# Optimization experiments

Hardware: AMD Instinct MI355X
Metric: run time of the kernel (lower is better)

## Reference

```python
import jax, jax.numpy as jnp
import numpy as np

EPS = 1e-5  # torch BatchNorm2d default eps


def setup_inputs() -> dict:
    key = jax.random.key(0)
    ks = jax.random.split(key, 11)
    n, c, h, w = 16, 512, 64, 64
    grp, cg, mip = 4, 128, 16
    return {
        "x": jax.random.normal(ks[0], (n, c, h, w), dtype=jnp.float32),
        "W1": jax.random.normal(ks[1], (mip, cg), dtype=jnp.float32) * 0.05,
        "b1": jax.random.normal(ks[2], (mip,), dtype=jnp.float32) * 0.05,
        "gamma": jax.random.uniform(ks[3], (mip,), dtype=jnp.float32, minval=0.5, maxval=1.5),
        "beta": jax.random.normal(ks[4], (mip,), dtype=jnp.float32) * 0.05,
        "mean": jax.random.normal(ks[5], (mip,), dtype=jnp.float32) * 0.05,
        "var": jax.random.uniform(ks[6], (mip,), dtype=jnp.float32, minval=0.5, maxval=1.5),
        "Wh": jax.random.normal(ks[7], (cg, mip), dtype=jnp.float32) * 0.1,
        "bh": jax.random.normal(ks[8], (cg,), dtype=jnp.float32) * 0.05,
        "Ww": jax.random.normal(ks[9], (cg, mip), dtype=jnp.float32) * 0.1,
        "bw": jax.random.normal(ks[10], (cg,), dtype=jnp.float32) * 0.05,
    }


def reference(x, W1, b1, gamma, beta, mean, var, Wh, bh, Ww, bw):
    n, c, h, w = x.shape
    grp = 4
    cg = c // grp
    # Since c % 4 == 0, torch.split gives 4 equal groups: fold group into a new axis.
    xg = x.reshape(n, grp, cg, h, w)                       # (n,g,cg,h,w)
    gh = xg.mean(axis=4)                                   # pool over w -> (n,g,cg,h)
    gw = xg.mean(axis=3)                                   # pool over h -> (n,g,cg,w)
    y = jnp.concatenate([gh, gw], axis=3)                  # (n,g,cg,h+w)
    # conv1 (1x1) shared across all 4 groups
    y = jnp.einsum('ngcl,mc->ngml', y, W1) + b1[None, None, :, None]
    # BatchNorm2d (eval mode, running stats)
    scale = gamma / jnp.sqrt(var + EPS)
    y = y * scale[None, None, :, None] + (beta - mean * scale)[None, None, :, None]
    # h_swish: x * relu6(x+3)/6
    y = y * (jnp.clip(y + 3.0, 0.0, 6.0) / 6.0)
    yh, yw = y[..., :h], y[..., h:]                        # (n,g,mip,h), (n,g,mip,w)
    a_h = jax.nn.sigmoid(jnp.einsum('ngml,cm->ngcl', yh, Wh) + bh[None, None, :, None])
    a_w = jax.nn.sigmoid(jnp.einsum('ngml,cm->ngcl', yw, Ww) + bw[None, None, :, None])
    out = xg * a_h[..., :, None] * a_w[..., None, :]       # (n,g,cg,h,w)
    out = out.reshape(n, c, h, w)
    # channel shuffle: (n, cg, grp, h, w) -> permute group axis forward
    out = out.reshape(n, cg, grp, h, w).transpose(0, 2, 1, 3, 4).reshape(n, c, h, w)
    return out
```

## Files before the change

### kernel.cpp

```cpp
#include <hip/hip_runtime.h>

#define N_   16
#define C_   512
#define H_   64
#define W_   64
#define GRP  4
#define CG   128
#define MIP  16

__device__ __forceinline__ float bf_lo(unsigned u) { return __uint_as_float(u << 16); }
__device__ __forceinline__ float bf_hi(unsigned u) { return __uint_as_float(u & 0xFFFF0000u); }
__device__ __forceinline__ float bf1(unsigned short s) { return __uint_as_float((unsigned)s << 16); }

__device__ __forceinline__ float ld_scalar(const void* p, int i, bool isbf) {
    return isbf ? bf1(((const unsigned short*)p)[i]) : ((const float*)p)[i];
}

__device__ __forceinline__ bool sniff_isbf(const unsigned* __restrict__ x32,
                                           int t, unsigned* s_flag) {
    if (t < 64) {
        int cnt = 0;
        #pragma unroll
        for (int k = 0; k < 4; ++k) {
            unsigned w = x32[t + 64 * k];
            unsigned e = (w >> 7) & 0xFFu;
            cnt += (e >= 0x60u && e <= 0x9Fu) ? 1 : 0;
        }
        #pragma unroll
        for (int off = 32; off > 0; off >>= 1) cnt += __shfl_down(cnt, off, 64);
        if (t == 0) *s_flag = (cnt >= 192) ? 1u : 0u;
    }
    __syncthreads();
    return *s_flag != 0u;
}

__global__ __launch_bounds__(256) void kreduce(const void* __restrict__ xv,
                                               float* __restrict__ gh,
                                               float* __restrict__ gw) {
    __shared__ float tile[64 * 65];
    __shared__ unsigned flag_s;
    const int bid = blockIdx.x;
    const int t = threadIdx.x;
    const bool isbf = sniff_isbf((const unsigned*)xv, t, &flag_s);

    if (isbf) {
        const uint4* src = (const uint4*)((const unsigned short*)xv + (size_t)bid * 4096);
        #pragma unroll
        for (int half = 0; half < 2; ++half) {
            int idx = t + half * 256;
            int r = idx >> 3;
            int j0 = (idx & 7) * 8;
            uint4 v = src[idx];
            unsigned uu[4] = {v.x, v.y, v.z, v.w};
            #pragma unroll
            for (int k = 0; k < 4; ++k) {
                tile[r * 65 + j0 + 2 * k]     = bf_lo(uu[k]);
                tile[r * 65 + j0 + 2 * k + 1] = bf_hi(uu[k]);
            }
        }
    } else {
        const float4* src = (const float4*)((const float*)xv + (size_t)bid * 4096);
        #pragma unroll
        for (int it = 0; it < 4; ++it) {
            int idx = t + it * 256;
            int r = idx >> 4;
            int j0 = (idx & 15) * 4;
            float4 v = src[idx];
            tile[r * 65 + j0]     = v.x;
            tile[r * 65 + j0 + 1] = v.y;
            tile[r * 65 + j0 + 2] = v.z;
            tile[r * 65 + j0 + 3] = v.w;
        }
    }
    __syncthreads();

    if (t < 64) {
        float s = 0.f;
        #pragma unroll
        for (int j = 0; j < 64; ++j) s += tile[t * 65 + j];
        gh[(size_t)bid * 64 + t] = s * (1.0f / 64.0f);
    } else if (t < 128) {
        int j = t - 64;
        float s = 0.f;
        #pragma unroll
        for (int i = 0; i < 64; ++i) s += tile[i * 65 + j];
        gw[(size_t)bid * 64 + j] = s * (1.0f / 64.0f);
    }
}

__global__ __launch_bounds__(256) void ky(
    const void* __restrict__ xv,
    const float* __restrict__ gh, const float* __restrict__ gw,
    const void* __restrict__ W1, const void* __restrict__ b1,
    const void* __restrict__ gamma, const void* __restrict__ beta,
    const void* __restrict__ mean, const void* __restrict__ var,
    float* __restrict__ y)
{
    __shared__ float W1_s[MIP * CG];
    __shared__ float scale_s[MIP], shift_s[MIP], b1_s[MIP];
    __shared__ unsigned flag_s;

    const int t = threadIdx.x;
    const bool isbf = sniff_isbf((const unsigned*)xv, t, &flag_s);

    if (isbf) {
        uint4 v = ((const uint4*)W1)[t];
        unsigned uu[4] = {v.x, v.y, v.z, v.w};
        #pragma unroll
        for (int k = 0; k < 4; ++k) {
            W1_s[t * 8 + 2 * k]     = bf_lo(uu[k]);
            W1_s[t * 8 + 2 * k + 1] = bf_hi(uu[k]);
        }
    } else {
        #pragma unroll
        for (int it = 0; it < 2; ++it) {
            int idx = t + 256 * it;
            float4 v = ((const float4*)W1)[idx];
            W1_s[idx * 4]     = v.x;
            W1_s[idx * 4 + 1] = v.y;
            W1_s[idx * 4 + 2] = v.z;
            W1_s[idx * 4 + 3] = v.w;
        }
    }
    if (t < MIP) {
        float sc = ld_scalar(gamma, t, isbf) * rsqrtf(ld_scalar(var, t, isbf) + 1e-5f);
        scale_s[t] = sc;
        shift_s[t] = ld_scalar(beta, t, isbf) - ld_scalar(mean, t, isbf) * sc;
        b1_s[t] = ld_scalar(b1, t, isbf);
    }
    __syncthreads();

    const int l = t & 127;
    const int half = t >> 7;
    const size_t base = (size_t)blockIdx.x * (CG * 64);
    const float* src = (l < 64) ? (gh + base + l) : (gw + base + (l - 64));
    float acc[8] = {0.f, 0.f, 0.f, 0.f, 0.f, 0.f, 0.f, 0.f};
    for (int cc = 0; cc < CG; ++cc) {
        float v = src[(size_t)cc * 64];
        #pragma unroll
        for (int mm = 0; mm < 8; ++mm)
            acc[mm] += W1_s[(half * 8 + mm) * CG + cc] * v;
    }
    float* yb = y + (size_t)blockIdx.x * (MIP * 128);
    #pragma unroll
    for (int mm = 0; mm < 8; ++mm) {
        int m = half * 8 + mm;
        float yv = acc[mm] + b1_s[m];
        yv = yv * scale_s[m] + shift_s[m];
        float hc = fminf(fmaxf(yv + 3.0f, 0.0f), 6.0f);
        yb[m * 128 + l] = yv * hc * (1.0f / 6.0f);
    }
}

__global__ __launch_bounds__(256) void kapply(const void* __restrict__ xv,
                                              const float* __restrict__ y,
                                              const void* __restrict__ Wh,
                                              const void* __restrict__ bh,
                                              const void* __restrict__ Ww,
                                              const void* __restrict__ bw,
                                              void* __restrict__ outv) {
    __shared__ float ah_s[64], aw_s[64];
    __shared__ unsigned flag_s;
    const int bid = blockIdx.x;
    const int n = bid >> 9;
    const int o = bid & 511;
    const int g2 = o >> 7, cc2 = o & 127;
    const int p = cc2 * 4 + g2;
    const int g = p >> 7, cc = p & 127;
    const int t = threadIdx.x;
    const bool isbf = sniff_isbf((const unsigned*)xv, t, &flag_s);

    if (t < 128) {
        const int i = t & 63;
        const bool isW = (t >= 64);
        const void* Wp = isW ? Ww : Wh;
        const void* bp = isW ? bw : bh;
        const float* ysrc = y + (size_t)(n * 4 + g) * (MIP * 128) + (isW ? 64 : 0) + i;
        float acc = ld_scalar(bp, cc, isbf);
        #pragma unroll
        for (int m = 0; m < MIP; ++m)
            acc += ld_scalar(Wp, cc * MIP + m, isbf) * ysrc[m * 128];
        float s = 1.0f / (1.0f + __expf(-acc));
        if (isW) aw_s[i] = s; else ah_s[i] = s;
    }
    __syncthreads();

    if (isbf) {
        const uint4* src = (const uint4*)((const unsigned short*)xv + ((size_t)n * 512 + p) * 4096);
        uint4* dst = (uint4*)((unsigned short*)outv + (size_t)bid * 4096);
        #pragma unroll
        for (int half = 0; half < 2; ++half) {
            int idx = t + half * 256;
            int r = idx >> 3;
            int j0 = (idx & 7) * 8;
            float sah = ah_s[r];
            uint4 v = src[idx];
            unsigned uu[4] = {v.x, v.y, v.z, v.w};
            unsigned res[4];
            #pragma unroll
            for (int k = 0; k < 4; ++k) {
                int j = j0 + 2 * k;
                float f0 = bf_lo(uu[k]) * sah * aw_s[j];
                float f1 = bf_hi(uu[k]) * sah * aw_s[j + 1];
                unsigned u0 = __float_as_uint(f0); u0 += 0x7FFFu + ((u0 >> 16) & 1u);
                unsigned u1 = __float_as_uint(f1); u1 += 0x7FFFu + ((u1 >> 16) & 1u);
                res[k] = (u0 >> 16) | (u1 & 0xFFFF0000u);
            }
            uint4 w; w.x = res[0]; w.y = res[1]; w.z = res[2]; w.w = res[3];
            dst[idx] = w;
        }
    } else {
        const float4* src = (const float4*)((const float*)xv + ((size_t)n * 512 + p) * 4096);
        float4* dst = (float4*)((float*)outv + (size_t)bid * 4096);
        #pragma unroll
        for (int it = 0; it < 4; ++it) {
            int idx = t + it * 256;
            int r = idx >> 4;
            int j0 = (idx & 15) * 4;
            float sah = ah_s[r];
            float4 v = src[idx];
            v.x *= sah * aw_s[j0];
            v.y *= sah * aw_s[j0 + 1];
            v.z *= sah * aw_s[j0 + 2];
            v.w *= sah * aw_s[j0 + 3];
            dst[idx] = v;
        }
    }
}

extern "C" void kernel_launch(void* const* d_in, const int* in_sizes, int n_in,
                              void* d_out, int out_size, void* d_ws, size_t ws_size,
                              hipStream_t stream) {
    const void* x     = d_in[0];
    const void* W1    = d_in[1];
    const void* b1    = d_in[2];
    const void* gamma = d_in[3];
    const void* beta  = d_in[4];
    const void* mean  = d_in[5];
    const void* var   = d_in[6];
    const void* Wh    = d_in[7];
    const void* bh    = d_in[8];
    const void* Ww    = d_in[9];
    const void* bw    = d_in[10];

    float* ws = (float*)d_ws;
    const size_t seg = (size_t)N_ * GRP * CG * 64;
    float* gh = ws;
    float* gw = gh + seg;
    float* yv = gw + seg;

    kreduce<<<N_ * C_, 256, 0, stream>>>(x, gh, gw);
    ky<<<N_ * GRP, 256, 0, stream>>>(x, gh, gw, W1, b1, gamma, beta, mean, var, yv);
    kapply<<<N_ * C_, 256, 0, stream>>>(x, yv, Wh, bh, Ww, bw, d_out);
}
```

Before: 277.7 us.

## Move attention sigmoid into mid kernel and reduce pools with register shuffles

The reduce kernel now builds row sums with wavefront shuffles and column partials in registers, instead of staging the whole 64x64 tile in shared memory and reducing it serially. The second-stage conv plus sigmoid moves from the apply kernel into the 64-block mid kernel, which writes precomputed a_h/a_w arrays, so each apply block only loads 128 floats. The apply kernel also issues its x loads before the barrier to overlap them with the attention fetch. The mid kernel now does more serial work on only 64 blocks, which could lengthen that stage.

After: 291.1 us. 4.8% more time.

```diff
diff --git a/kernel.cpp b/kernel.cpp
--- a/kernel.cpp
+++ b/kernel.cpp
@@ -2,8 +2,6 @@
 
 #define N_   16
 #define C_   512
-#define H_   64
-#define W_   64
 #define GRP  4
 #define CG   128
 #define MIP  16
@@ -37,7 +35,7 @@
 __global__ __launch_bounds__(256) void kreduce(const void* __restrict__ xv,
                                                float* __restrict__ gh,
                                                float* __restrict__ gw) {
-    __shared__ float tile[64 * 65];
+    __shared__ float scratch[32][65];
     __shared__ unsigned flag_s;
     const int bid = blockIdx.x;
     const int t = threadIdx.x;
@@ -45,62 +43,74 @@
 
     if (isbf) {
         const uint4* src = (const uint4*)((const unsigned short*)xv + (size_t)bid * 4096);
-        #pragma unroll
-        for (int half = 0; half < 2; ++half) {
-            int idx = t + half * 256;
+        float cp[8] = {0,0,0,0,0,0,0,0};
+        #pragma unroll
+        for (int hf = 0; hf < 2; ++hf) {
+            int idx = t + hf * 256;
             int r = idx >> 3;
-            int j0 = (idx & 7) * 8;
             uint4 v = src[idx];
             unsigned uu[4] = {v.x, v.y, v.z, v.w};
+            float rp = 0.f;
             #pragma unroll
             for (int k = 0; k < 4; ++k) {
-                tile[r * 65 + j0 + 2 * k]     = bf_lo(uu[k]);
-                tile[r * 65 + j0 + 2 * k + 1] = bf_hi(uu[k]);
+                float f0 = bf_lo(uu[k]), f1 = bf_hi(uu[k]);
+                rp += f0 + f1;
+                cp[2*k] += f0; cp[2*k+1] += f1;
             }
-        }
+            rp += __shfl_xor(rp, 1);
+            rp += __shfl_xor(rp, 2);
+            rp += __shfl_xor(rp, 4);
+            if ((t & 7) == 0) gh[(size_t)bid * 64 + r] = rp * (1.f/64.f);
+        }
+        #pragma unroll
+        for (int k = 0; k < 8; ++k) scratch[t >> 3][(t & 7) * 8 + k] = cp[k];
     } else {
         const float4* src = (const float4*)((const float*)xv + (size_t)bid * 4096);
+        float cp[4] = {0,0,0,0};
         #pragma unroll
         for (int it = 0; it < 4; ++it) {
             int idx = t + it * 256;
             int r = idx >> 4;
-            int j0 = (idx & 15) * 4;
             float4 v = src[idx];
-            tile[r * 65 + j0]     = v.x;
-            tile[r * 65 + j0 + 1] = v.y;
-            tile[r * 65 + j0 + 2] = v.z;
-            tile[r * 65 + j0 + 3] = v.w;
-        }
-    }
-    __syncthreads();
-
+            float rp = (v.x + v.y) + (v.z + v.w);
+            cp[0] += v.x; cp[1] += v.y; cp[2] += v.z; cp[3] += v.w;
+            rp += __shfl_xor(rp, 1);
+            rp += __shfl_xor(rp, 2);
+            rp += __shfl_xor(rp, 4);
+            rp += __shfl_xor(rp, 8);
+            if ((t & 15) == 0) gh[(size_t)bid * 64 + r] = rp * (1.f/64.f);
+        }
+        #pragma unroll
+        for (int k = 0; k < 4; ++k) scratch[t >> 4][(t & 15) * 4 + k] = cp[k];
+    }
+    __syncthreads();
     if (t < 64) {
+        const int nr = isbf ? 32 : 16;
         float s = 0.f;
-        #pragma unroll
-        for (int j = 0; j < 64; ++j) s += tile[t * 65 + j];
-        gh[(size_t)bid * 64 + t] = s * (1.0f / 64.0f);
-    } else if (t < 128) {
-        int j = t - 64;
-        float s = 0.f;
-        #pragma unroll
-        for (int i = 0; i < 64; ++i) s += tile[i * 65 + j];
-        gw[(size_t)bid * 64 + j] = s * (1.0f / 64.0f);
-    }
-}
-
-__global__ __launch_bounds__(256) void ky(
+        for (int i = 0; i < nr; ++i) s += scratch[i][t];
+        gw[(size_t)bid * 64 + t] = s * (1.f/64.f);
+    }
+}
+
+__global__ __launch_bounds__(256) void kmid(
     const void* __restrict__ xv,
     const float* __restrict__ gh, const float* __restrict__ gw,
     const void* __restrict__ W1, const void* __restrict__ b1,
     const void* __restrict__ gamma, const void* __restrict__ beta,
     const void* __restrict__ mean, const void* __restrict__ var,
-    float* __restrict__ y)
+    const void* __restrict__ Wh, const void* __restrict__ bh,
+    const void* __restrict__ Ww, const void* __restrict__ bw,
+    float* __restrict__ aH, float* __restrict__ aW)
 {
     __shared__ float W1_s[MIP * CG];
+    __shared__ float Whw_s[2][CG * MIP];
+    __shared__ float y_s[MIP * 128];
+    __shared__ float bhw_s[2][CG];
     __shared__ float scale_s[MIP], shift_s[MIP], b1_s[MIP];
     __shared__ unsigned flag_s;
 
     const int t = threadIdx.x;
+    const int ng = blockIdx.x;
     const bool isbf = sniff_isbf((const unsigned*)xv, t, &flag_s);
 
     if (isbf) {
@@ -108,20 +118,37 @@
         unsigned uu[4] = {v.x, v.y, v.z, v.w};
         #pragma unroll
         for (int k = 0; k < 4; ++k) {
-            W1_s[t * 8 + 2 * k]     = bf_lo(uu[k]);
-            W1_s[t * 8 + 2 * k + 1] = bf_hi(uu[k]);
+            W1_s[t*8 + 2*k]   = bf_lo(uu[k]);
+            W1_s[t*8 + 2*k+1] = bf_hi(uu[k]);
+        }
+        uint4 a = ((const uint4*)Wh)[t];
+        unsigned ua[4] = {a.x, a.y, a.z, a.w};
+        #pragma unroll
+        for (int k = 0; k < 4; ++k) {
+            Whw_s[0][t*8 + 2*k]   = bf_lo(ua[k]);
+            Whw_s[0][t*8 + 2*k+1] = bf_hi(ua[k]);
+        }
+        uint4 c = ((const uint4*)Ww)[t];
+        unsigned uc[4] = {c.x, c.y, c.z, c.w};
+        #pragma unroll
+        for (int k = 0; k < 4; ++k) {
+            Whw_s[1][t*8 + 2*k]   = bf_lo(uc[k]);
+            Whw_s[1][t*8 + 2*k+1] = bf_hi(uc[k]);
         }
     } else {
         #pragma unroll
         for (int it = 0; it < 2; ++it) {
             int idx = t + 256 * it;
             float4 v = ((const float4*)W1)[idx];
-            W1_s[idx * 4]     = v.x;
-            W1_s[idx * 4 + 1] = v.y;
-            W1_s[idx * 4 + 2] = v.z;
-            W1_s[idx * 4 + 3] = v.w;
-        }
-    }
+            W1_s[idx*4] = v.x; W1_s[idx*4+1] = v.y; W1_s[idx*4+2] = v.z; W1_s[idx*4+3] = v.w;
+            float4 a = ((const float4*)Wh)[idx];
+            Whw_s[0][idx*4] = a.x; Whw_s[0][idx*4+1] = a.y; Whw_s[0][idx*4+2] = a.z; Whw_s[0][idx*4+3] = a.w;
+            float4 c = ((const float4*)Ww)[idx];
+            Whw_s[1][idx*4] = c.x; Whw_s[1][idx*4+1] = c.y; Whw_s[1][idx*4+2] = c.z; Whw_s[1][idx*4+3] = c.w;
+        }
+    }
+    if (t < CG) bhw_s[0][t] = ld_scalar(bh, t, isbf);
+    else        bhw_s[1][t - CG] = ld_scalar(bw, t - CG, isbf);
     if (t < MIP) {
         float sc = ld_scalar(gamma, t, isbf) * rsqrtf(ld_scalar(var, t, isbf) + 1e-5f);
         scale_s[t] = sc;
@@ -130,72 +157,75 @@
     }
     __syncthreads();
 
-    const int l = t & 127;
-    const int half = t >> 7;
-    const size_t base = (size_t)blockIdx.x * (CG * 64);
-    const float* src = (l < 64) ? (gh + base + l) : (gw + base + (l - 64));
-    float acc[8] = {0.f, 0.f, 0.f, 0.f, 0.f, 0.f, 0.f, 0.f};
-    for (int cc = 0; cc < CG; ++cc) {
-        float v = src[(size_t)cc * 64];
-        #pragma unroll
-        for (int mm = 0; mm < 8; ++mm)
-            acc[mm] += W1_s[(half * 8 + mm) * CG + cc] * v;
-    }
-    float* yb = y + (size_t)blockIdx.x * (MIP * 128);
-    #pragma unroll
-    for (int mm = 0; mm < 8; ++mm) {
-        int m = half * 8 + mm;
-        float yv = acc[mm] + b1_s[m];
-        yv = yv * scale_s[m] + shift_s[m];
-        float hc = fminf(fmaxf(yv + 3.0f, 0.0f), 6.0f);
-        yb[m * 128 + l] = yv * hc * (1.0f / 6.0f);
+    {
+        const int l = t & 127;
+        const int half = t >> 7;
+        const float* gbase = (l < 64) ? (gh + (size_t)ng * 8192 + l)
+                                      : (gw + (size_t)ng * 8192 + (l - 64));
+        float acc[8] = {0,0,0,0,0,0,0,0};
+        for (int cc = 0; cc < CG; ++cc) {
+            float v = gbase[(size_t)cc * 64];
+            #pragma unroll
+            for (int mm = 0; mm < 8; ++mm)
+                acc[mm] += W1_s[(half*8 + mm) * CG + cc] * v;
+        }
+        #pragma unroll
+        for (int mm = 0; mm < 8; ++mm) {
+            int m = half*8 + mm;
+            float yv = acc[mm] + b1_s[m];
+            yv = yv * scale_s[m] + shift_s[m];
+            float hc = fminf(fmaxf(yv + 3.f, 0.f), 6.f);
+            y_s[m * 128 + l] = yv * hc * (1.f/6.f);
+        }
+    }
+    __syncthreads();
+
+    for (int k = 0; k < 64; ++k) {
+        int out = t + 256 * k;
+        int hf = out >> 13;
+        int rem = out & 8191;
+        int cc = rem >> 6;
+        int i = rem & 63;
+        float acc = bhw_s[hf][cc];
+        #pragma unroll
+        for (int m = 0; m < MIP; ++m)
+            acc += Whw_s[hf][cc * MIP + m] * y_s[m * 128 + hf * 64 + i];
+        float s = 1.f / (1.f + __expf(-acc));
+        float* dst = hf ? aW : aH;
+        dst[(size_t)ng * 8192 + cc * 64 + i] = s;
     }
 }
 
 __global__ __launch_bounds__(256) void kapply(const void* __restrict__ xv,
-                                              const float* __restrict__ y,
-                                              const void* __restrict__ Wh,
-                                              const void* __restrict__ bh,
-                                              const void* __restrict__ Ww,
-                                              const void* __restrict__ bw,
+                                              const float* __restrict__ aH,
+                                              const float* __restrict__ aW,
                                               void* __restrict__ outv) {
     __shared__ float ah_s[64], aw_s[64];
     __shared__ unsigned flag_s;
     const int bid = blockIdx.x;
     const int n = bid >> 9;
     const int o = bid & 511;
-    const int g2 = o >> 7, cc2 = o & 127;
-    const int p = cc2 * 4 + g2;
+    const int p = (o & 127) * 4 + (o >> 7);
     const int g = p >> 7, cc = p & 127;
     const int t = threadIdx.x;
     const bool isbf = sniff_isbf((const unsigned*)xv, t, &flag_s);
-
-    if (t < 128) {
-        const int i = t & 63;
-        const bool isW = (t >= 64);
-        const void* Wp = isW ? Ww : Wh;
-        const void* bp = isW ? bw : bh;
-        const float* ysrc = y + (size_t)(n * 4 + g) * (MIP * 128) + (isW ? 64 : 0) + i;
-        float acc = ld_scalar(bp, cc, isbf);
-        #pragma unroll
-        for (int m = 0; m < MIP; ++m)
-            acc += ld_scalar(Wp, cc * MIP + m, isbf) * ysrc[m * 128];
-        float s = 1.0f / (1.0f + __expf(-acc));
-        if (isW) aw_s[i] = s; else ah_s[i] = s;
-    }
-    __syncthreads();
+    const size_t abase = (size_t)(n * 4 + g) * 8192 + (size_t)cc * 64;
 
     if (isbf) {
         const uint4* src = (const uint4*)((const unsigned short*)xv + ((size_t)n * 512 + p) * 4096);
+        uint4 x0 = src[t];
+        uint4 x1 = src[t + 256];
+        if (t < 64)       ah_s[t]      = aH[abase + t];
+        else if (t < 128) aw_s[t - 64] = aW[abase + (t - 64)];
+        __syncthreads();
         uint4* dst = (uint4*)((unsigned short*)outv + (size_t)bid * 4096);
-        #pragma unroll
-        for (int half = 0; half < 2; ++half) {
-            int idx = t + half * 256;
-            int r = idx >> 3;
-            int j0 = (idx & 7) * 8;
+        uint4 xr[2] = {x0, x1};
+        #pragma unroll
+        for (int hf = 0; hf < 2; ++hf) {
+            int idx = t + hf * 256;
+            int r = idx >> 3, j0 = (idx & 7) * 8;
             float sah = ah_s[r];
-            uint4 v = src[idx];
-            unsigned uu[4] = {v.x, v.y, v.z, v.w};
+            unsigned uu[4] = {xr[hf].x, xr[hf].y, xr[hf].z, xr[hf].w};
             unsigned res[4];
             #pragma unroll
             for (int k = 0; k < 4; ++k) {
@@ -206,19 +236,26 @@
                 unsigned u1 = __float_as_uint(f1); u1 += 0x7FFFu + ((u1 >> 16) & 1u);
                 res[k] = (u0 >> 16) | (u1 & 0xFFFF0000u);
             }
-            uint4 w; w.x = res[0]; w.y = res[1]; w.z = res[2]; w.w = res[3];
-            dst[idx] = w;
+            uint4 w2; w2.x = res[0]; w2.y = res[1]; w2.z = res[2]; w2.w = res[3];
+            dst[idx] = w2;
         }
     } else {
         const float4* src = (const float4*)((const float*)xv + ((size_t)n * 512 + p) * 4096);
+        float4 x0 = src[t];
+        float4 x1 = src[t + 256];
+        float4 x2 = src[t + 512];
+        float4 x3 = src[t + 768];
+        if (t < 64)       ah_s[t]      = aH[abase + t];
+        else if (t < 128) aw_s[t - 64] = aW[abase + (t - 64)];
+        __syncthreads();
         float4* dst = (float4*)((float*)outv + (size_t)bid * 4096);
+        float4 xr[4] = {x0, x1, x2, x3};
         #pragma unroll
         for (int it = 0; it < 4; ++it) {
             int idx = t + it * 256;
-            int r = idx >> 4;
-            int j0 = (idx & 15) * 4;
+            int r = idx >> 4, j0 = (idx & 15) * 4;
             float sah = ah_s[r];
-            float4 v = src[idx];
+            float4 v = xr[it];
             v.x *= sah * aw_s[j0];
             v.y *= sah * aw_s[j0 + 1];
             v.z *= sah * aw_s[j0 + 2];
@@ -244,12 +281,13 @@
     const void* bw    = d_in[10];
 
     float* ws = (float*)d_ws;
-    const size_t seg = (size_t)N_ * GRP * CG * 64;
     float* gh = ws;
-    float* gw = gh + seg;
-    float* yv = gw + seg;
+    float* gw = gh + 524288;
+    float* aH = gw + 524288;
+    float* aW = aH + 524288;
 
     kreduce<<<N_ * C_, 256, 0, stream>>>(x, gh, gw);
-    ky<<<N_ * GRP, 256, 0, stream>>>(x, gh, gw, W1, b1, gamma, beta, mean, var, yv);
-    kapply<<<N_ * C_, 256, 0, stream>>>(x, yv, Wh, bh, Ww, bw, d_out);
-}
+    kmid<<<N_ * GRP, 256, 0, stream>>>(x, gh, gw, W1, b1, gamma, beta, mean, var,
+                                       Wh, bh, Ww, bw, aH, aW);
+    kapply<<<N_ * C_, 256, 0, stream>>>(x, aH, aW, d_out);
+}
```
